# Optimization experiments

Measured on AMD Instinct MI355X. Metric: run time of the kernel, lower is better.

The kernel has to match this reference:

```python
import jax, jax.numpy as jnp
import numpy as np

DT = 0.1  # module init arg dt


def _skew(v):
    x, y, z = v[..., 0], v[..., 1], v[..., 2]
    o = jnp.zeros_like(x)
    return jnp.stack([
        jnp.stack([o, -z, y], -1),
        jnp.stack([z, o, -x], -1),
        jnp.stack([-y, x, o], -1)], -2)


def _se3_exp(xi):
    # pypose se3 convention: [tau (trans), phi (rot)]
    tau, phi = xi[..., :3], xi[..., 3:6]
    th2 = jnp.sum(phi * phi, -1)
    th = jnp.sqrt(th2)
    small = th < 1e-4
    ts = jnp.where(small, 1.0, th)
    A = jnp.where(small, 1.0 - th2 / 6.0, jnp.sin(ts) / ts)
    B = jnp.where(small, 0.5 - th2 / 24.0, (1.0 - jnp.cos(ts)) / (ts * ts))
    C = jnp.where(small, 1.0 / 6.0 - th2 / 120.0, (ts - jnp.sin(ts)) / (ts ** 3))
    K = _skew(phi)
    K2 = K @ K
    I = jnp.eye(3, dtype=xi.dtype)
    R = I + A[..., None, None] * K + B[..., None, None] * K2
    V = I + B[..., None, None] * K + C[..., None, None] * K2
    t = jnp.einsum('...ij,...j->...i', V, tau)
    return R, t


def _so3_log(R):
    tr = R[..., 0, 0] + R[..., 1, 1] + R[..., 2, 2]
    c = jnp.clip((tr - 1.0) * 0.5, -1.0 + 1e-7, 1.0 - 1e-7)
    th = jnp.arccos(c)
    small = th < 1e-4
    ts = jnp.where(small, 1.0, th)
    coef = jnp.where(small, 0.5 + th * th / 12.0, ts / (2.0 * jnp.sin(ts)))
    W = coef[..., None, None] * (R - jnp.swapaxes(R, -1, -2))
    return jnp.stack([W[..., 2, 1], W[..., 0, 2], W[..., 1, 0]], -1), th


def _se3_log(R, t):
    phi, th = _so3_log(R)
    th2 = th * th
    small = th < 1e-4
    ts = jnp.where(small, 1.0, th)
    # V^{-1} coefficient: (1 - th*sin(th)/(2*(1-cos(th))))/th^2, Taylor 1/12 + th^2/720
    D = jnp.where(small, 1.0 / 12.0 + th2 / 720.0,
                  (1.0 - ts * jnp.sin(ts) / (2.0 * (1.0 - jnp.cos(ts)))) / (ts * ts))
    K = _skew(phi)
    K2 = K @ K
    I = jnp.eye(3, dtype=R.dtype)
    Vinv = I - 0.5 * K + D[..., None, None] * K2
    tau = jnp.einsum('...ij,...j->...i', Vinv, t)
    return jnp.concatenate([tau, phi], -1)


def _compose(a, b):
    Ra, ta = a
    Rb, tb = b
    return Ra @ Rb, jnp.einsum('...ij,...j->...i', Ra, tb) + ta


def _inv(a):
    R, t = a
    Rt = jnp.swapaxes(R, -1, -2)
    return Rt, -jnp.einsum('...ij,...j->...i', Rt, t)


def _kinematic_consistency(x, dt):
    x_t = x[..., :-1, :]
    x_t_dt = x[..., 1:, :]
    H_t = _se3_exp(x_t[..., :6])
    fwd = _compose(_se3_exp(x_t[..., 6:] * (dt / 2.0)), H_t)
    H_t_dt = _se3_exp(x_t_dt[..., :6])
    bwd = _compose(_se3_exp(x_t_dt[..., 6:] * (-dt / 2.0)), H_t_dt)
    Rd, td = _compose(fwd, _inv(bwd))
    xi = _se3_log(Rd, td)
    return jnp.linalg.norm(xi, axis=-1)  # [B, H-1]


def setup_inputs() -> dict:
    key = jax.random.key(0)
    k1, k2, k3, k4 = jax.random.split(key, 4)
    traj = jax.random.normal(k1, (8192, 128, 12), jnp.float32)
    k = jax.random.randint(k2, (8192,), 0, 1000)
    t_weights = jax.random.uniform(k3, (127,), jnp.float32)
    k_weights = jax.random.uniform(k4, (1000,), jnp.float32)
    return {"traj": traj, "k": k, "t_weights": t_weights, "k_weights": k_weights}


def reference(traj, k, t_weights, k_weights):
    score = _kinematic_consistency(traj, DT)
    loss = score * score  # mse vs zeros, reduction='none'
    weighted = (loss * t_weights).mean(axis=1) * k_weights[k]  # [B]
    return weighted.mean()
```

## Files before the change

kernel.cpp:

```cpp
#include <hip/hip_runtime.h>
#include <math.h>

#define DEV __device__ __forceinline__

DEV float fast_rcp(float x) { return __builtin_amdgcn_rcpf(x); }

DEV float fast_acos(float x) {
    float ax = fabsf(x);
    float p = fmaf(ax, -0.0187293f, 0.0742610f);
    p = fmaf(ax, p, -0.2121144f);
    p = fmaf(ax, p, 1.5707288f);
    float r = sqrtf(1.0f - ax) * p;
    return (x < 0.0f) ? (3.14159265358979f - r) : r;
}

DEV void se3_exp(float tau0, float tau1, float tau2,
                 float x, float y, float z,
                 float R[9], float t[3]) {
    float th2 = x*x + y*y + z*z;
    float th  = sqrtf(th2);
    bool small = th < 1e-4f;
    float ts  = small ? 1.0f : th;
    float s   = __sinf(ts);
    float c   = __cosf(ts);
    float inv = fast_rcp(ts);
    float A = small ? (1.0f - th2 * (1.0f/6.0f))      : s * inv;
    float B = small ? (0.5f - th2 * (1.0f/24.0f))     : (1.0f - c) * inv * inv;
    float C = small ? (1.0f/6.0f - th2*(1.0f/120.0f)) : (ts - s) * inv * inv * inv;

    float Bxy = B*x*y, Bxz = B*x*z, Byz = B*y*z;
    R[0] = 1.0f - B*(y*y + z*z);
    R[1] = Bxy - A*z;
    R[2] = Bxz + A*y;
    R[3] = Bxy + A*z;
    R[4] = 1.0f - B*(x*x + z*z);
    R[5] = Byz - A*x;
    R[6] = Bxz - A*y;
    R[7] = Byz + A*x;
    R[8] = 1.0f - B*(x*x + y*y);

    float Cxy = C*x*y, Cxz = C*x*z, Cyz = C*y*z;
    float V0 = 1.0f - C*(y*y + z*z);
    float V1 = Cxy - B*z;
    float V2 = Cxz + B*y;
    float V3 = Cxy + B*z;
    float V4 = 1.0f - C*(x*x + z*z);
    float V5 = Cyz - B*x;
    float V6 = Cxz - B*y;
    float V7 = Cyz + B*x;
    float V8 = 1.0f - C*(x*x + y*y);
    t[0] = V0*tau0 + V1*tau1 + V2*tau2;
    t[1] = V3*tau0 + V4*tau1 + V5*tau2;
    t[2] = V6*tau0 + V7*tau1 + V8*tau2;
}

DEV void make_fwd_bwd(const float Rp[9], const float tp[3],
                      const float Rv[9], const float tv[3],
                      float F[12], float Bw[12]) {
    #pragma unroll
    for (int i = 0; i < 3; i++)
        #pragma unroll
        for (int j = 0; j < 3; j++) {
            F[i*3+j]  = Rv[i*3+0]*Rp[0*3+j] + Rv[i*3+1]*Rp[1*3+j] + Rv[i*3+2]*Rp[2*3+j];
            Bw[i*3+j] = Rv[0*3+i]*Rp[0*3+j] + Rv[1*3+i]*Rp[1*3+j] + Rv[2*3+i]*Rp[2*3+j];
        }
    float d0 = tp[0]-tv[0], d1 = tp[1]-tv[1], d2 = tp[2]-tv[2];
    #pragma unroll
    for (int i = 0; i < 3; i++) {
        F[9+i]  = Rv[i*3+0]*tp[0] + Rv[i*3+1]*tp[1] + Rv[i*3+2]*tp[2] + tv[i];
        Bw[9+i] = Rv[0*3+i]*d0 + Rv[1*3+i]*d1 + Rv[2*3+i]*d2;
    }
}

DEV float pair_loss(const float F[12], const float B[12]) {
    float Rd[9];
    #pragma unroll
    for (int i = 0; i < 3; i++)
        #pragma unroll
        for (int j = 0; j < 3; j++)
            Rd[i*3+j] = F[i*3+0]*B[j*3+0] + F[i*3+1]*B[j*3+1] + F[i*3+2]*B[j*3+2];
    float td0 = F[9]  - (Rd[0]*B[9] + Rd[1]*B[10] + Rd[2]*B[11]);
    float td1 = F[10] - (Rd[3]*B[9] + Rd[4]*B[10] + Rd[5]*B[11]);
    float td2 = F[11] - (Rd[6]*B[9] + Rd[7]*B[10] + Rd[8]*B[11]);

    float tr = Rd[0] + Rd[4] + Rd[8];
    float c  = fminf(fmaxf((tr - 1.0f) * 0.5f, -1.0f + 1e-7f), 1.0f - 1e-7f);
    float th = fast_acos(c);
    float sn = sqrtf(fmaxf(1.0f - c*c, 1e-20f));
    float coef = th * fast_rcp(2.0f * sn);
    float px = coef * (Rd[7] - Rd[5]);
    float py = coef * (Rd[2] - Rd[6]);
    float pz = coef * (Rd[3] - Rd[1]);

    float D = (1.0f - th*sn*fast_rcp(2.0f*(1.0f - c))) * fast_rcp(th*th);
    float Dxy = D*px*py, Dxz = D*px*pz, Dyz = D*py*pz;
    float Vi0 = 1.0f - D*(py*py + pz*pz);
    float Vi1 = Dxy + 0.5f*pz;
    float Vi2 = Dxz - 0.5f*py;
    float Vi3 = Dxy - 0.5f*pz;
    float Vi4 = 1.0f - D*(px*px + pz*pz);
    float Vi5 = Dyz + 0.5f*px;
    float Vi6 = Dxz + 0.5f*py;
    float Vi7 = Dyz - 0.5f*px;
    float Vi8 = 1.0f - D*(px*px + py*py);
    float ux = Vi0*td0 + Vi1*td1 + Vi2*td2;
    float uy = Vi3*td0 + Vi4*td1 + Vi5*td2;
    float uz = Vi6*td0 + Vi7*td1 + Vi8*td2;

    return ux*ux + uy*uy + uz*uz + px*px + py*py + pz*pz;
}

__global__ __launch_bounds__(256)
void kin_kernel(const float* __restrict__ traj, const int* __restrict__ kidx,
                const float* __restrict__ tw, const float* __restrict__ kw,
                float* __restrict__ partial) {
    const int tid     = threadIdx.x;
    const int lane    = tid & 63;
    const int traj_id = blockIdx.x * 4 + (tid >> 6);

    const float* base = traj + (size_t)traj_id * 1536 + lane * 24;
    float4 a0 = *(const float4*)(base + 0);
    float4 a1 = *(const float4*)(base + 4);
    float4 a2 = *(const float4*)(base + 8);
    float4 b0 = *(const float4*)(base + 12);
    float4 b1 = *(const float4*)(base + 16);
    float4 b2 = *(const float4*)(base + 20);

    float kwv = kw[kidx[traj_id]];
    float w0  = tw[2*lane];
    float w1  = (lane < 63) ? tw[2*lane + 1] : 0.0f;

    const float h = 0.05f;
    float Rp[9], tp[3], Rv[9], tv[3];

    se3_exp(a0.x,a0.y,a0.z, a0.w,a1.x,a1.y, Rp, tp);
    se3_exp(a1.z*h,a1.w*h,a2.x*h, a2.y*h,a2.z*h,a2.w*h, Rv, tv);
    float FA[12], BA[12];
    make_fwd_bwd(Rp,tp,Rv,tv, FA,BA);

    float RB[12];
    #pragma unroll
    for (int i = 0; i < 12; i++) RB[i] = __shfl_down(BA[i], 1, 64);

    se3_exp(b0.x,b0.y,b0.z, b0.w,b1.x,b1.y, Rp, tp);
    se3_exp(b1.z*h,b1.w*h,b2.x*h, b2.y*h,b2.z*h,b2.w*h, Rv, tv);
    float FB[12], BB[12];
    make_fwd_bwd(Rp,tp,Rv,tv, FB,BB);

    float term = pair_loss(FA, BB) * w0;
    if (lane < 63) term += pair_loss(FB, RB) * w1;

    #pragma unroll
    for (int off = 32; off; off >>= 1) term += __shfl_down(term, off, 64);
    if (lane == 0) partial[traj_id] = term * kwv;
}

__global__ __launch_bounds__(512)
void reduce_kernel(const float4* __restrict__ partial4, float* __restrict__ out,
                   int n4, float scale) {
    __shared__ float ws[8];
    int tid = threadIdx.x;
    float v = 0.0f;
    for (int i = tid; i < n4; i += 512) {
        float4 p = partial4[i];
        v += (p.x + p.y) + (p.z + p.w);
    }
    #pragma unroll
    for (int off = 32; off; off >>= 1) v += __shfl_down(v, off, 64);
    if ((tid & 63) == 0) ws[tid >> 6] = v;
    __syncthreads();
    if (tid == 0) {
        float s = 0.0f;
        #pragma unroll
        for (int i = 0; i < 8; i++) s += ws[i];
        out[0] = s * scale;
    }
}

extern "C" void kernel_launch(void* const* d_in, const int* in_sizes, int n_in,
                              void* d_out, int out_size, void* d_ws, size_t ws_size,
                              hipStream_t stream) {
    const float* traj = (const float*)d_in[0];
    const int*   k    = (const int*)d_in[1];
    const float* tw   = (const float*)d_in[2];
    const float* kw   = (const float*)d_in[3];
    float* out     = (float*)d_out;
    float* partial = (float*)d_ws;
    const int B = in_sizes[1];

    kin_kernel<<<B / 4, 256, 0, stream>>>(traj, k, tw, kw, partial);
    float scale = 1.0f / (127.0f * (float)B);
    reduce_kernel<<<1, 512, 0, stream>>>((const float4*)partial, out, B / 4, scale);
}
```

Measured before the change: 96.05 us.

## Stage trajectory loads through LDS for coalesced global reads

Each wave now reads its 128x12 trajectory with fully coalesced float4 loads (consecutive lanes read consecutive float4s) instead of per-lane 96-byte strided chunks. It transposes the data into a padded LDS buffer in a column layout, then reads each lane's two timesteps from LDS. Launch bounds also request 5 blocks per SM to cap register use. This adds LDS traffic, a block-level sync and some occupancy pressure from about 25KB of LDS per block.

```diff
diff --git a/kernel.cpp b/kernel.cpp
--- a/kernel.cpp
+++ b/kernel.cpp
@@ -110,42 +110,60 @@
     return ux*ux + uy*uy + uz*uz + px*px + py*py + pz*pz;
 }
 
-__global__ __launch_bounds__(256)
+#define CS 132
+__global__ __launch_bounds__(256, 5)
 void kin_kernel(const float* __restrict__ traj, const int* __restrict__ kidx,
                 const float* __restrict__ tw, const float* __restrict__ kw,
                 float* __restrict__ partial) {
+    __shared__ float lds[4][12 * CS];
     const int tid     = threadIdx.x;
     const int lane    = tid & 63;
-    const int traj_id = blockIdx.x * 4 + (tid >> 6);
-
-    const float* base = traj + (size_t)traj_id * 1536 + lane * 24;
-    float4 a0 = *(const float4*)(base + 0);
-    float4 a1 = *(const float4*)(base + 4);
-    float4 a2 = *(const float4*)(base + 8);
-    float4 b0 = *(const float4*)(base + 12);
-    float4 b1 = *(const float4*)(base + 16);
-    float4 b2 = *(const float4*)(base + 20);
+    const int wave    = tid >> 6;
+    const int traj_id = blockIdx.x * 4 + wave;
+
+    float* W = lds[wave];
+    const float4* g = (const float4*)(traj + (size_t)traj_id * 1536);
+    #pragma unroll
+    for (int i = 0; i < 6; i++) {
+        int f = lane + 64 * i;
+        float4 v = g[f];
+        int r     = f / 3;
+        int cb    = (f - r * 3) * 4;
+        int slot  = (r >> 1) + ((r & 1) << 6);
+        W[(cb + 0) * CS + slot] = v.x;
+        W[(cb + 1) * CS + slot] = v.y;
+        W[(cb + 2) * CS + slot] = v.z;
+        W[(cb + 3) * CS + slot] = v.w;
+    }
+    __syncthreads();
 
     float kwv = kw[kidx[traj_id]];
-    float w0  = tw[2*lane];
-    float w1  = (lane < 63) ? tw[2*lane + 1] : 0.0f;
+    float w0  = tw[2 * lane];
+    float w1  = (lane < 63) ? tw[2 * lane + 1] : 0.0f;
+
+    float a[12], bq[12];
+    #pragma unroll
+    for (int c = 0; c < 12; c++) {
+        a[c]  = W[c * CS + lane];
+        bq[c] = W[c * CS + 64 + lane];
+    }
 
     const float h = 0.05f;
     float Rp[9], tp[3], Rv[9], tv[3];
 
-    se3_exp(a0.x,a0.y,a0.z, a0.w,a1.x,a1.y, Rp, tp);
-    se3_exp(a1.z*h,a1.w*h,a2.x*h, a2.y*h,a2.z*h,a2.w*h, Rv, tv);
+    se3_exp(a[0],a[1],a[2], a[3],a[4],a[5], Rp, tp);
+    se3_exp(a[6]*h,a[7]*h,a[8]*h, a[9]*h,a[10]*h,a[11]*h, Rv, tv);
     float FA[12], BA[12];
-    make_fwd_bwd(Rp,tp,Rv,tv, FA,BA);
+    make_fwd_bwd(Rp, tp, Rv, tv, FA, BA);
 
     float RB[12];
     #pragma unroll
     for (int i = 0; i < 12; i++) RB[i] = __shfl_down(BA[i], 1, 64);
 
-    se3_exp(b0.x,b0.y,b0.z, b0.w,b1.x,b1.y, Rp, tp);
-    se3_exp(b1.z*h,b1.w*h,b2.x*h, b2.y*h,b2.z*h,b2.w*h, Rv, tv);
+    se3_exp(bq[0],bq[1],bq[2], bq[3],bq[4],bq[5], Rp, tp);
+    se3_exp(bq[6]*h,bq[7]*h,bq[8]*h, bq[9]*h,bq[10]*h,bq[11]*h, Rv, tv);
     float FB[12], BB[12];
-    make_fwd_bwd(Rp,tp,Rv,tv, FB,BB);
+    make_fwd_bwd(Rp, tp, Rv, tv, FB, BB);
 
     float term = pair_loss(FA, BB) * w0;
     if (lane < 63) term += pair_loss(FB, RB) * w1;
```

New measurement: 112.9 us. +17.6%, slower.
